# Kernel tuning notes

Measured on AMD Instinct MI355X. Metric: run time of the kernel, lower is better.

Reference implementation:

```python
import jax, jax.numpy as jnp
import numpy as np

B, S, HID, NH = 2, 2048, 2048, 16
DH = HID // NH  # 128


def _rope_tables(seq_len, dim, dtype=jnp.float32):
    inv_freq = 1.0 / (10000.0 ** (jnp.arange(0, dim, 2, dtype=jnp.float32) / dim))
    t = jnp.arange(seq_len, dtype=jnp.float32)
    freqs = jnp.einsum('i,j->ij', t, inv_freq)          # [S, dim/2]
    emb = jnp.concatenate([freqs, freqs], axis=-1)       # [S, dim]
    return jnp.cos(emb)[None, None].astype(dtype), jnp.sin(emb)[None, None].astype(dtype)


def _rotate_half(x):
    x1, x2 = x[..., : x.shape[-1] // 2], x[..., x.shape[-1] // 2 :]
    return jnp.concatenate([-x2, x1], axis=-1)


def setup_inputs() -> dict:
    key = jax.random.key(0)
    ks = jax.random.split(key, 6)
    hidden_states = jax.random.normal(ks[0], (B, S, HID), dtype=jnp.float32)
    scale = 1.0 / np.sqrt(HID)
    Wq = jax.random.normal(ks[1], (HID, HID), dtype=jnp.float32) * scale
    Wk = jax.random.normal(ks[2], (HID, HID), dtype=jnp.float32) * scale
    Wv = jax.random.normal(ks[3], (HID, HID), dtype=jnp.float32) * scale
    Wo = jax.random.normal(ks[4], (HID, HID), dtype=jnp.float32) * scale
    bq = jnp.zeros((HID,), jnp.float32)
    bk = jnp.zeros((HID,), jnp.float32)
    bv = jnp.zeros((HID,), jnp.float32)
    bo = jnp.zeros((HID,), jnp.float32)
    # causal additive mask [1,1,S,S]
    causal = jnp.tril(jnp.ones((S, S), dtype=bool))
    attention_mask = jnp.where(causal, 0.0, -1e9).astype(jnp.float32)[None, None]
    return dict(hidden_states=hidden_states, attention_mask=attention_mask,
                Wq=Wq, bq=bq, Wk=Wk, bk=bk, Wv=Wv, bv=bv, Wo=Wo, bo=bo)


def reference(hidden_states, attention_mask, Wq, bq, Wk, bk, Wv, bv, Wo, bo):
    b, s, _ = hidden_states.shape
    # torch Linear: x @ W.T + b
    q = (hidden_states @ Wq.T + bq).reshape(b, s, NH, DH).transpose(0, 2, 1, 3)
    k = (hidden_states @ Wk.T + bk).reshape(b, s, NH, DH).transpose(0, 2, 1, 3)
    v = (hidden_states @ Wv.T + bv).reshape(b, s, NH, DH).transpose(0, 2, 1, 3)
    cos, sin = _rope_tables(s, DH)
    q = q * cos + _rotate_half(q) * sin
    k = k * cos + _rotate_half(k) * sin
    scores = jnp.einsum('bhqd,bhkd->bhqk', q * (DH ** -0.5), k)
    scores = scores + attention_mask
    probs = jax.nn.softmax(scores, axis=-1)  # dropout: eval mode (identity)
    out = jnp.einsum('bhqk,bhkd->bhqd', probs, v)
    out = out.transpose(0, 2, 1, 3).reshape(b, s, HID)
    return out @ Wo.T + bo
```

## Files before the change

### kernel.cpp

```cpp
#include <hip/hip_runtime.h>
#include <hip/hip_bf16.h>
#include <cstdint>
#include <cstddef>

#define BB 2
#define SS 2048
#define HH 2048
#define NHH 16
#define DHH 128

using f32x4  = __attribute__((ext_vector_type(4))) float;
using bf16x8 = __attribute__((ext_vector_type(8))) __bf16;
using bf16x4 = __attribute__((ext_vector_type(4))) __bf16;
using bfloat = __bf16;

__device__ inline void gload_lds16(const void* g, void* l) {
    __builtin_amdgcn_global_load_lds(
        (const __attribute__((address_space(1))) void*)g,
        (__attribute__((address_space(3))) void*)l, 16, 0, 0);
}

__device__ inline f32x4 mfma16(bf16x8 a, bf16x8 b, f32x4 c) {
    return __builtin_amdgcn_mfma_f32_16x16x32_bf16(a, b, c, 0, 0, 0);
}

template <int CTRL>
__device__ inline float dpp_max_step(float x) {
    int y = __builtin_amdgcn_update_dpp(0, __builtin_bit_cast(int, x), CTRL, 0xf, 0xf, false);
    return fmaxf(x, __builtin_bit_cast(float, y));
}
__device__ inline float rowmax16(float x) {
    x = dpp_max_step<0x121>(x);
    x = dpp_max_step<0x122>(x);
    x = dpp_max_step<0x124>(x);
    x = dpp_max_step<0x128>(x);
    return x;
}

__global__ void cvt_bf16(const float* __restrict__ in, bfloat* __restrict__ out, int n4) {
    int i = blockIdx.x * blockDim.x + threadIdx.x;
    if (i >= n4) return;
    float4 v = reinterpret_cast<const float4*>(in)[i];
    bf16x4 o;
    o[0] = (bfloat)v.x; o[1] = (bfloat)v.y; o[2] = (bfloat)v.z; o[3] = (bfloat)v.w;
    reinterpret_cast<bf16x4*>(out)[i] = o;
}

__global__ void cvt_bf16_w(const float* __restrict__ s0, const float* __restrict__ s1,
                           const float* __restrict__ s2, const float* __restrict__ s3,
                           bfloat* __restrict__ d0, bfloat* __restrict__ d1,
                           bfloat* __restrict__ d2, bfloat* __restrict__ d3) {
    int sel = blockIdx.x >> 12;
    int i = (blockIdx.x & 4095) * 256 + threadIdx.x;
    const float* s = sel == 0 ? s0 : sel == 1 ? s1 : sel == 2 ? s2 : s3;
    bfloat* d = sel == 0 ? d0 : sel == 1 ? d1 : sel == 2 ? d2 : d3;
    float4 v = reinterpret_cast<const float4*>(s)[i];
    bf16x4 o;
    o[0] = (bfloat)v.x; o[1] = (bfloat)v.y; o[2] = (bfloat)v.z; o[3] = (bfloat)v.w;
    reinterpret_cast<bf16x4*>(d)[i] = o;
}

__global__ void rope_table(float* __restrict__ cosT, float* __restrict__ sinT) {
    int i = blockIdx.x * blockDim.x + threadIdx.x;
    if (i >= SS * 64) return;
    int s = i >> 6, j = i & 63;
    float invf = powf(10000.0f, -(float)j / 64.0f);
    float ang = (float)s * invf;
    cosT[i] = cosf(ang);
    sinT[i] = sinf(ang);
}

__global__ __launch_bounds__(256, 2)
void gemm_qkv(const bfloat* __restrict__ A,
              const bfloat* __restrict__ Bq, const bfloat* __restrict__ Bk,
              const bfloat* __restrict__ Bv,
              const float* __restrict__ bq, const float* __restrict__ bk,
              const float* __restrict__ bv,
              bfloat* __restrict__ Qo, bfloat* __restrict__ Ko, bfloat* __restrict__ Vto,
              const float* __restrict__ cosT, const float* __restrict__ sinT) {
    constexpr int BM = 128, BN = 128, BK = 32, K = HH, N = HH;
    __shared__ bfloat As[BM * BK];
    __shared__ bfloat Bs[BN * BK];
    const int t = threadIdx.x, w = t >> 6, l = t & 63;
    const int lr = l & 15, lg = l >> 4;
    const int sel = blockIdx.y >> 4;
    const bfloat* Bt = sel == 0 ? Bq : sel == 1 ? Bk : Bv;
    const float* bias = sel == 0 ? bq : sel == 1 ? bk : bv;
    const int m0 = blockIdx.x * BM, n0 = (blockIdx.y & 15) * BN;
    const int wm = (w >> 1) * 64;
    const int base = (t & ~63) * 8;

    f32x4 acc[4][4] = {};

    for (int kb = 0; kb < K; kb += BK) {
#pragma unroll
        for (int i = 0; i < 2; i++) {
            int idx = i * 256 + t;
            int r = idx >> 2, k8 = (idx & 3) << 3;
            gload_lds16(A  + (size_t)(m0 + r) * K + kb + k8, As + (i * 2048 + base));
            gload_lds16(Bt + (size_t)(n0 + r) * K + kb + k8, Bs + (i * 2048 + base));
        }
        __syncthreads();
        bf16x8 af[4], bfr[4];
#pragma unroll
        for (int mi = 0; mi < 4; mi++)
            af[mi] = *reinterpret_cast<const bf16x8*>(&As[(wm + mi * 16 + lr) * BK + lg * 8]);
#pragma unroll
        for (int ni = 0; ni < 4; ni++) {
            int cb = (w & 1) * 32 + (ni & 1) * 16 + (ni >> 1) * 64;
            bfr[ni] = *reinterpret_cast<const bf16x8*>(&Bs[(cb + lr) * BK + lg * 8]);
        }
#pragma unroll
        for (int mi = 0; mi < 4; mi++)
#pragma unroll
            for (int ni = 0; ni < 4; ni++)
                acc[mi][ni] = mfma16(af[mi], bfr[ni], acc[mi][ni]);
        __syncthreads();
    }

    if (sel == 2) {
#pragma unroll
        for (int mi = 0; mi < 4; mi++) {
            int row = m0 + wm + mi * 16 + lg * 4;
#pragma unroll
            for (int ni = 0; ni < 4; ni++) {
                int cb = (w & 1) * 32 + (ni & 1) * 16 + (ni >> 1) * 64;
                int col = n0 + cb + lr;
                float bv_ = bias[col];
#pragma unroll
                for (int j = 0; j < 4; j++) {
                    float v = acc[mi][ni][j] + bv_;
                    int bb = (row + j) >> 11;
                    int s  = (row + j) & (SS - 1);
                    Vto[((size_t)(bb * HH + col)) * SS + s] = (bfloat)v;
                }
            }
        }
    } else {
        bfloat* C = sel == 0 ? Qo : Ko;
        const float qscale = sel == 0 ? 0.088388347648318447f : 1.0f;
#pragma unroll
        for (int mi = 0; mi < 4; mi++) {
            int row = m0 + wm + mi * 16 + lg * 4;
#pragma unroll
            for (int ni = 0; ni < 2; ni++) {
                int d = (w & 1) * 32 + ni * 16 + lr;
                int col1 = n0 + d, col2 = col1 + 64;
                float b1 = bias[col1], b2 = bias[col2];
#pragma unroll
                for (int j = 0; j < 4; j++) {
                    int s = (row + j) & (SS - 1);
                    float c  = cosT[s * 64 + d];
                    float sn = sinT[s * 64 + d];
                    float x1 = acc[mi][ni][j] + b1;
                    float x2 = acc[mi][ni + 2][j] + b2;
                    float o1 = (x1 * c - x2 * sn) * qscale;
                    float o2 = (x2 * c + x1 * sn) * qscale;
                    C[(size_t)(row + j) * N + col1] = (bfloat)o1;
                    C[(size_t)(row + j) * N + col2] = (bfloat)o2;
                }
            }
        }
    }
}

__global__ __launch_bounds__(256, 2)
void gemm_out(const bfloat* __restrict__ A, const bfloat* __restrict__ Bt,
              const float* __restrict__ bias, float* __restrict__ C,
              int M, int N, int K) {
    constexpr int BM = 128, BN = 128, BK = 32;
    __shared__ bfloat As[BM * BK];
    __shared__ bfloat Bs[BN * BK];
    const int t = threadIdx.x, w = t >> 6, l = t & 63;
    const int lr = l & 15, lg = l >> 4;
    const int m0 = blockIdx.x * BM, n0 = blockIdx.y * BN;
    const int wm = (w >> 1) * 64;
    const int base = (t & ~63) * 8;

    f32x4 acc[4][4] = {};

    for (int kb = 0; kb < K; kb += BK) {
#pragma unroll
        for (int i = 0; i < 2; i++) {
            int idx = i * 256 + t;
            int r = idx >> 2, k8 = (idx & 3) << 3;
            gload_lds16(A  + (size_t)(m0 + r) * K + kb + k8, As + (i * 2048 + base));
            gload_lds16(Bt + (size_t)(n0 + r) * K + kb + k8, Bs + (i * 2048 + base));
        }
        __syncthreads();
        bf16x8 af[4], bfr[4];
#pragma unroll
        for (int mi = 0; mi < 4; mi++)
            af[mi] = *reinterpret_cast<const bf16x8*>(&As[(wm + mi * 16 + lr) * BK + lg * 8]);
#pragma unroll
        for (int ni = 0; ni < 4; ni++) {
            int cb = (w & 1) * 32 + (ni & 1) * 16 + (ni >> 1) * 64;
            bfr[ni] = *reinterpret_cast<const bf16x8*>(&Bs[(cb + lr) * BK + lg * 8]);
        }
#pragma unroll
        for (int mi = 0; mi < 4; mi++)
#pragma unroll
            for (int ni = 0; ni < 4; ni++)
                acc[mi][ni] = mfma16(af[mi], bfr[ni], acc[mi][ni]);
        __syncthreads();
    }

#pragma unroll
    for (int mi = 0; mi < 4; mi++) {
        int row = m0 + wm + mi * 16 + lg * 4;
#pragma unroll
        for (int ni = 0; ni < 4; ni++) {
            int cb = (w & 1) * 32 + (ni & 1) * 16 + (ni >> 1) * 64;
            int col = n0 + cb + lr;
            float bv = bias[col];
#pragma unroll
            for (int j = 0; j < 4; j++)
                C[(size_t)(row + j) * N + col] = acc[mi][ni][j] + bv;
        }
    }
}

__global__ __launch_bounds__(256, 4)
void attn_fwd(const bfloat* __restrict__ Q, const bfloat* __restrict__ K,
              const bfloat* __restrict__ Vt, bfloat* __restrict__ O) {
    __shared__ bfloat Ks[64 * 128];
    __shared__ bfloat Vs[128 * 64];
    __shared__ bfloat Pw[4][16 * 64];

    const int t = threadIdx.x, w = t >> 6, l = t & 63;
    const int lr = l & 15, lg = l >> 4;
    const int swz = (lr & 7) << 4;

    const int f = blockIdx.x;
    const int xcd = f & 7, slot = f >> 3;
    const int bh = xcd + 8 * (slot >> 5);
    const int qidx = 31 - (slot & 31);
    const int b = bh >> 4, h = bh & 15;
    const int q0 = qidx * 64 + w * 16;

    const size_t bo_ = (size_t)b * SS * HH + (size_t)h * DHH;
    const bfloat* Qp = Q + bo_;
    const bfloat* Kp = K + bo_;
    const bfloat* Vp = Vt + (size_t)(b * NHH + h) * DHH * SS;
    bfloat* Op = O + bo_;

    auto stage = [&](int kv0) {
#pragma unroll
        for (int i = 0; i < 4; i++) {
            int Ub = (i * 4 + w) * 64;
            int U = Ub + l;
            int r = U >> 4;
            int u = (U & 15) ^ (r & 7);
            gload_lds16(Kp + (size_t)(kv0 + r) * HH + u * 8, &Ks[Ub * 8]);
        }
#pragma unroll
        for (int i = 0; i < 4; i++) {
            int Ub = (i * 4 + w) * 64;
            int U = Ub + l;
            int r = U >> 3;
            int u = (U & 7) ^ (r & 7);
            gload_lds16(Vp + (size_t)r * SS + kv0 + u * 8, &Vs[Ub * 8]);
        }
    };

    bf16x8 qf[4];
#pragma unroll
    for (int kt = 0; kt < 4; kt++)
        qf[kt] = *reinterpret_cast<const bf16x8*>(Qp + (size_t)(q0 + lr) * HH + kt * 32 + lg * 8);

    bf16x8 ones;
#pragma unroll
    for (int e = 0; e < 8; e++) ones[e] = (bfloat)1.0f;

    f32x4 o[8] = {};
    f32x4 lsv = {};
    float m[4];
#pragma unroll
    for (int j = 0; j < 4; j++) m[j] = -1e30f;

    const int nkv = qidx + 1;

    for (int kv = 0; kv < nkv; ++kv) {
        stage(kv * 64);
        __syncthreads();

        const char* KB = (const char*)&Ks[0];
        const char* VB = (const char*)&Vs[0];

        f32x4 sc[4] = {};
        __builtin_amdgcn_s_setprio(1);
#pragma unroll
        for (int kt = 0; kt < 4; kt++) {
            const int col = (kt * 64 + lg * 16);
#pragma unroll
            for (int kb = 0; kb < 4; kb++) {
                bf16x8 kf = *reinterpret_cast<const bf16x8*>(
                    KB + (kb * 16 + lr) * 256 + (col ^ swz));
                sc[kb] = mfma16(qf[kt], kf, sc[kb]);
            }
        }
        __builtin_amdgcn_s_setprio(0);

        const bool diag = (kv == nkv - 1);
        float p[4][4], alpha[4];
        bool ga = false;
#pragma unroll
        for (int j = 0; j < 4; j++) {
            float v0 = sc[0][j], v1 = sc[1][j], v2 = sc[2][j], v3 = sc[3][j];
            if (diag) {
                int qr = q0 + lg * 4 + j;
                int k0 = kv * 64 + lr;
                if (k0      > qr) v0 = -1e30f;
                if (k0 + 16 > qr) v1 = -1e30f;
                if (k0 + 32 > qr) v2 = -1e30f;
                if (k0 + 48 > qr) v3 = -1e30f;
            }
            float mx = rowmax16(fmaxf(fmaxf(v0, v1), fmaxf(v2, v3)));
            bool grow = mx > m[j] + 8.0f;
            float mn = grow ? mx : m[j];
            alpha[j] = grow ? __expf(m[j] - mn) : 1.0f;
            m[j] = mn;
            ga = ga || grow;
            p[0][j] = __expf(v0 - mn);
            p[1][j] = __expf(v1 - mn);
            p[2][j] = __expf(v2 - mn);
            p[3][j] = __expf(v3 - mn);
        }
        if (__any(ga)) {
#pragma unroll
            for (int j = 0; j < 4; j++) {
                lsv[j] *= alpha[j];
#pragma unroll
                for (int nt = 0; nt < 8; nt++) o[nt][j] *= alpha[j];
            }
        }

        char* pwb = (char*)&Pw[w][0];
#pragma unroll
        for (int j = 0; j < 4; j++) {
            int q = lg * 4 + j;
            int qs = (q & 7) << 4;
#pragma unroll
            for (int kb = 0; kb < 4; kb++)
                *(bfloat*)(pwb + q * 128 + ((kb * 32 + lr * 2) ^ qs)) = (bfloat)p[kb][j];
        }
        asm volatile("s_waitcnt lgkmcnt(0)" ::: "memory");
        __builtin_amdgcn_sched_barrier(0);

        const char* pwr = (const char*)&Pw[w][0];
        bf16x8 pa0 = *reinterpret_cast<const bf16x8*>(pwr + lr * 128 + ((lg * 16) ^ swz));
        bf16x8 pa1 = *reinterpret_cast<const bf16x8*>(pwr + lr * 128 + ((64 + lg * 16) ^ swz));
        __builtin_amdgcn_s_setprio(1);
        lsv = mfma16(pa0, ones, lsv);
        lsv = mfma16(pa1, ones, lsv);
#pragma unroll
        for (int nt = 0; nt < 8; nt++) {
            const char* vb = VB + (nt * 16 + lr) * 128;
            bf16x8 vf0 = *reinterpret_cast<const bf16x8*>(vb + ((lg * 16) ^ swz));
            bf16x8 vf1 = *reinterpret_cast<const bf16x8*>(vb + ((64 + lg * 16) ^ swz));
            o[nt] = mfma16(pa0, vf0, o[nt]);
            o[nt] = mfma16(pa1, vf1, o[nt]);
        }
        __builtin_amdgcn_s_setprio(0);
        __syncthreads();
    }

#pragma unroll
    for (int j = 0; j < 4; j++) {
        float inv = 1.0f / lsv[j];
        int row = q0 + lg * 4 + j;
#pragma unroll
        for (int nt = 0; nt < 8; nt++)
            Op[(size_t)row * HH + nt * 16 + lr] = (bfloat)(o[nt][j] * inv);
    }
}

extern "C" void kernel_launch(void* const* d_in, const int* in_sizes, int n_in,
                              void* d_out, int out_size, void* d_ws, size_t ws_size,
                              hipStream_t stream) {
    (void)in_sizes; (void)n_in; (void)out_size; (void)ws_size;
    const float* hs = (const float*)d_in[0];
    const float* Wq = (const float*)d_in[2];
    const float* bq = (const float*)d_in[3];
    const float* Wk = (const float*)d_in[4];
    const float* bk = (const float*)d_in[5];
    const float* Wv = (const float*)d_in[6];
    const float* bv = (const float*)d_in[7];
    const float* Wo = (const float*)d_in[8];
    const float* bo = (const float*)d_in[9];

    char* ws = (char*)d_ws;
    size_t off = 0;
    auto alloc = [&](size_t bytes) { void* p = ws + off; off += (bytes + 255) & ~(size_t)255; return p; };
    const size_t MK = (size_t)BB * SS * HH;
    const size_t NK = (size_t)HH * HH;

    bfloat* Xb  = (bfloat*)alloc(MK * 2);
    bfloat* Wqb = (bfloat*)alloc(NK * 2);
    bfloat* Wkb = (bfloat*)alloc(NK * 2);
    bfloat* Wvb = (bfloat*)alloc(NK * 2);
    bfloat* Wob = (bfloat*)alloc(NK * 2);
    bfloat* Qb  = (bfloat*)alloc(MK * 2);
    bfloat* Kb  = (bfloat*)alloc(MK * 2);
    bfloat* Vtb = (bfloat*)alloc(MK * 2);
    float*  cosT = (float*)alloc((size_t)SS * 64 * 4);
    float*  sinT = (float*)alloc((size_t)SS * 64 * 4);
    bfloat* AOb = Xb;

    cvt_bf16<<<(int)(MK / 4 / 256), 256, 0, stream>>>(hs, Xb, (int)(MK / 4));
    cvt_bf16_w<<<4 * 4096, 256, 0, stream>>>(Wq, Wk, Wv, Wo, Wqb, Wkb, Wvb, Wob);
    rope_table<<<(SS * 64 + 255) / 256, 256, 0, stream>>>(cosT, sinT);

    gemm_qkv<<<dim3(BB * SS / 128, 48), 256, 0, stream>>>(
        Xb, Wqb, Wkb, Wvb, bq, bk, bv, Qb, Kb, Vtb, cosT, sinT);

    attn_fwd<<<1024, 256, 0, stream>>>(Qb, Kb, Vtb, AOb);

    gemm_out<<<dim3(BB * SS / 128, HH / 128), 256, 0, stream>>>(
        AOb, Wob, bo, (float*)d_out, BB * SS, HH, HH);
}
```

Baseline: 308.8 us.

## Triple-buffer GEMM k-loop with 256x128 tiles, BK=64 and swizzled LDS

Replaces the single-buffered BK=32 GEMM main loop in both the QKV and output projections with a shared 3-stage pipelined k-loop. It uses 512-thread blocks computing 256x128 tiles, BK=64, and XOR-swizzled LDS layouts. Explicit vmcnt waits and barriers let global-to-LDS loads for later stages overlap the MFMA work of the current stage, and s_setprio raises priority during the MFMA burst. The cost is much more LDS per block (about 144KB), which limits occupancy, plus half as many blocks per grid.

```diff
diff --git a/kernel.cpp b/kernel.cpp
--- a/kernel.cpp
+++ b/kernel.cpp
@@ -70,7 +70,85 @@
     sinT[i] = sinf(ang);
 }
 
-__global__ __launch_bounds__(256, 2)
+__device__ __forceinline__ void kloop256(const bfloat* __restrict__ Ag,
+                                         const bfloat* __restrict__ Bg,
+                                         f32x4 (&acc)[4][4]) {
+    constexpr int K = HH, NT = K / 64;
+    __shared__ bfloat Abuf[3][256 * 64];
+    __shared__ bfloat Bbuf[3][128 * 64];
+    const int t = threadIdx.x, l = t & 63, lr = l & 15, lg = l >> 4;
+    const int wid = t >> 6, wr = wid >> 1, wc = wid & 1;
+    const int dstu = (t & ~63);
+
+    auto stage = [&](int buf, int kt) {
+#pragma unroll
+        for (int i = 0; i < 4; i++) {
+            int U = i * 512 + t, row = U >> 3, u = (U & 7) ^ (row & 7);
+            gload_lds16(Ag + (size_t)row * K + kt * 64 + u * 8,
+                        &Abuf[buf][(i * 512 + dstu) * 8]);
+        }
+#pragma unroll
+        for (int i = 0; i < 2; i++) {
+            int U = i * 512 + t, row = U >> 3, u = (U & 7) ^ (row & 7);
+            gload_lds16(Bg + (size_t)row * K + kt * 64 + u * 8,
+                        &Bbuf[buf][(i * 512 + dstu) * 8]);
+        }
+    };
+
+    int cmap[4];
+#pragma unroll
+    for (int n = 0; n < 4; n++)
+        cmap[n] = (n < 2) ? wc * 32 + n * 16 : 64 + wc * 32 + (n - 2) * 16;
+    const int usw0 = lg ^ (lr & 7);
+    const int usw1 = (4 + lg) ^ (lr & 7);
+
+    stage(0, 0);
+    stage(1, 1);
+
+#pragma unroll 1
+    for (int kt = 0; kt < NT; ++kt) {
+        const int buf = kt % 3;
+        if (kt + 2 < NT) {
+            stage((kt + 2) % 3, kt + 2);
+            asm volatile("s_waitcnt vmcnt(12)" ::: "memory");
+        } else if (kt + 1 < NT) {
+            asm volatile("s_waitcnt vmcnt(6)" ::: "memory");
+        } else {
+            asm volatile("s_waitcnt vmcnt(0)" ::: "memory");
+        }
+        __builtin_amdgcn_s_barrier();
+        __builtin_amdgcn_sched_barrier(0);
+
+        const bfloat* Ab = Abuf[buf];
+        const bfloat* Bb = Bbuf[buf];
+        bf16x8 af[4][2], bfr[4][2];
+#pragma unroll
+        for (int m = 0; m < 4; m++) {
+            int row = wr * 64 + m * 16 + lr;
+            af[m][0] = *reinterpret_cast<const bf16x8*>(&Ab[row * 64 + usw0 * 8]);
+            af[m][1] = *reinterpret_cast<const bf16x8*>(&Ab[row * 64 + usw1 * 8]);
+        }
+#pragma unroll
+        for (int n = 0; n < 4; n++) {
+            int row = cmap[n] + lr;
+            bfr[n][0] = *reinterpret_cast<const bf16x8*>(&Bb[row * 64 + usw0 * 8]);
+            bfr[n][1] = *reinterpret_cast<const bf16x8*>(&Bb[row * 64 + usw1 * 8]);
+        }
+        __builtin_amdgcn_s_setprio(1);
+#pragma unroll
+        for (int m = 0; m < 4; m++)
+#pragma unroll
+            for (int n = 0; n < 4; n++) {
+                acc[m][n] = mfma16(af[m][0], bfr[n][0], acc[m][n]);
+                acc[m][n] = mfma16(af[m][1], bfr[n][1], acc[m][n]);
+            }
+        __builtin_amdgcn_s_setprio(0);
+        __builtin_amdgcn_sched_barrier(0);
+        __builtin_amdgcn_s_barrier();
+    }
+}
+
+__global__ __launch_bounds__(512, 2)
 void gemm_qkv(const bfloat* __restrict__ A,
               const bfloat* __restrict__ Bq, const bfloat* __restrict__ Bk,
               const bfloat* __restrict__ Bv,
@@ -78,144 +156,83 @@
               const float* __restrict__ bv,
               bfloat* __restrict__ Qo, bfloat* __restrict__ Ko, bfloat* __restrict__ Vto,
               const float* __restrict__ cosT, const float* __restrict__ sinT) {
-    constexpr int BM = 128, BN = 128, BK = 32, K = HH, N = HH;
-    __shared__ bfloat As[BM * BK];
-    __shared__ bfloat Bs[BN * BK];
-    const int t = threadIdx.x, w = t >> 6, l = t & 63;
-    const int lr = l & 15, lg = l >> 4;
+    constexpr int K = HH, N = HH;
     const int sel = blockIdx.y >> 4;
     const bfloat* Bt = sel == 0 ? Bq : sel == 1 ? Bk : Bv;
     const float* bias = sel == 0 ? bq : sel == 1 ? bk : bv;
-    const int m0 = blockIdx.x * BM, n0 = (blockIdx.y & 15) * BN;
-    const int wm = (w >> 1) * 64;
-    const int base = (t & ~63) * 8;
+    const int m0 = blockIdx.x * 256, n0 = (blockIdx.y & 15) * 128;
 
     f32x4 acc[4][4] = {};
-
-    for (int kb = 0; kb < K; kb += BK) {
-#pragma unroll
-        for (int i = 0; i < 2; i++) {
-            int idx = i * 256 + t;
-            int r = idx >> 2, k8 = (idx & 3) << 3;
-            gload_lds16(A  + (size_t)(m0 + r) * K + kb + k8, As + (i * 2048 + base));
-            gload_lds16(Bt + (size_t)(n0 + r) * K + kb + k8, Bs + (i * 2048 + base));
-        }
-        __syncthreads();
-        bf16x8 af[4], bfr[4];
-#pragma unroll
-        for (int mi = 0; mi < 4; mi++)
-            af[mi] = *reinterpret_cast<const bf16x8*>(&As[(wm + mi * 16 + lr) * BK + lg * 8]);
-#pragma unroll
-        for (int ni = 0; ni < 4; ni++) {
-            int cb = (w & 1) * 32 + (ni & 1) * 16 + (ni >> 1) * 64;
-            bfr[ni] = *reinterpret_cast<const bf16x8*>(&Bs[(cb + lr) * BK + lg * 8]);
-        }
-#pragma unroll
-        for (int mi = 0; mi < 4; mi++)
-#pragma unroll
-            for (int ni = 0; ni < 4; ni++)
-                acc[mi][ni] = mfma16(af[mi], bfr[ni], acc[mi][ni]);
-        __syncthreads();
-    }
+    kloop256(A + (size_t)m0 * K, Bt + (size_t)n0 * K, acc);
+
+    const int t = threadIdx.x, l = t & 63, lr = l & 15, lg = l >> 4;
+    const int wid = t >> 6, wr = wid >> 1, wc = wid & 1;
 
     if (sel == 2) {
 #pragma unroll
-        for (int mi = 0; mi < 4; mi++) {
-            int row = m0 + wm + mi * 16 + lg * 4;
-#pragma unroll
-            for (int ni = 0; ni < 4; ni++) {
-                int cb = (w & 1) * 32 + (ni & 1) * 16 + (ni >> 1) * 64;
-                int col = n0 + cb + lr;
+        for (int m = 0; m < 4; m++) {
+            int row = m0 + wr * 64 + m * 16 + lg * 4;
+#pragma unroll
+            for (int n = 0; n < 4; n++) {
+                int cm = (n < 2) ? wc * 32 + n * 16 : 64 + wc * 32 + (n - 2) * 16;
+                int col = n0 + cm + lr;
                 float bv_ = bias[col];
 #pragma unroll
                 for (int j = 0; j < 4; j++) {
-                    float v = acc[mi][ni][j] + bv_;
-                    int bb = (row + j) >> 11;
-                    int s  = (row + j) & (SS - 1);
-                    Vto[((size_t)(bb * HH + col)) * SS + s] = (bfloat)v;
+                    int r = row + j;
+                    Vto[((size_t)((r >> 11) * HH + col)) * SS + (r & (SS - 1))] =
+                        (bfloat)(acc[m][n][j] + bv_);
                 }
             }
         }
     } else {
         bfloat* C = sel == 0 ? Qo : Ko;
-        const float qscale = sel == 0 ? 0.088388347648318447f : 1.0f;
-#pragma unroll
-        for (int mi = 0; mi < 4; mi++) {
-            int row = m0 + wm + mi * 16 + lg * 4;
-#pragma unroll
-            for (int ni = 0; ni < 2; ni++) {
-                int d = (w & 1) * 32 + ni * 16 + lr;
+        const float qs = sel == 0 ? 0.088388347648318447f : 1.0f;
+#pragma unroll
+        for (int m = 0; m < 4; m++) {
+            int row = m0 + wr * 64 + m * 16 + lg * 4;
+#pragma unroll
+            for (int n = 0; n < 2; n++) {
+                int d = wc * 32 + n * 16 + lr;
                 int col1 = n0 + d, col2 = col1 + 64;
                 float b1 = bias[col1], b2 = bias[col2];
 #pragma unroll
                 for (int j = 0; j < 4; j++) {
-                    int s = (row + j) & (SS - 1);
+                    int r = row + j, s = r & (SS - 1);
                     float c  = cosT[s * 64 + d];
                     float sn = sinT[s * 64 + d];
-                    float x1 = acc[mi][ni][j] + b1;
-                    float x2 = acc[mi][ni + 2][j] + b2;
-                    float o1 = (x1 * c - x2 * sn) * qscale;
-                    float o2 = (x2 * c + x1 * sn) * qscale;
-                    C[(size_t)(row + j) * N + col1] = (bfloat)o1;
-                    C[(size_t)(row + j) * N + col2] = (bfloat)o2;
+                    float x1 = acc[m][n][j] + b1;
+                    float x2 = acc[m][n + 2][j] + b2;
+                    C[(size_t)r * N + col1] = (bfloat)((x1 * c - x2 * sn) * qs);
+                    C[(size_t)r * N + col2] = (bfloat)((x2 * c + x1 * sn) * qs);
                 }
             }
         }
     }
 }
 
-__global__ __launch_bounds__(256, 2)
+__global__ __launch_bounds__(512, 2)
 void gemm_out(const bfloat* __restrict__ A, const bfloat* __restrict__ Bt,
-              const float* __restrict__ bias, float* __restrict__ C,
-              int M, int N, int K) {
-    constexpr int BM = 128, BN = 128, BK = 32;
-    __shared__ bfloat As[BM * BK];
-    __shared__ bfloat Bs[BN * BK];
-    const int t = threadIdx.x, w = t >> 6, l = t & 63;
-    const int lr = l & 15, lg = l >> 4;
-    const int m0 = blockIdx.x * BM, n0 = blockIdx.y * BN;
-    const int wm = (w >> 1) * 64;
-    const int base = (t & ~63) * 8;
+              const float* __restrict__ bias, float* __restrict__ C) {
+    constexpr int K = HH, N = HH;
+    const int m0 = blockIdx.x * 256, n0 = blockIdx.y * 128;
 
     f32x4 acc[4][4] = {};
-
-    for (int kb = 0; kb < K; kb += BK) {
-#pragma unroll
-        for (int i = 0; i < 2; i++) {
-            int idx = i * 256 + t;
-            int r = idx >> 2, k8 = (idx & 3) << 3;
-            gload_lds16(A  + (size_t)(m0 + r) * K + kb + k8, As + (i * 2048 + base));
-            gload_lds16(Bt + (size_t)(n0 + r) * K + kb + k8, Bs + (i * 2048 + base));
-        }
-        __syncthreads();
-        bf16x8 af[4], bfr[4];
-#pragma unroll
-        for (int mi = 0; mi < 4; mi++)
-            af[mi] = *reinterpret_cast<const bf16x8*>(&As[(wm + mi * 16 + lr) * BK + lg * 8]);
-#pragma unroll
-        for (int ni = 0; ni < 4; ni++) {
-            int cb = (w & 1) * 32 + (ni & 1) * 16 + (ni >> 1) * 64;
-            bfr[ni] = *reinterpret_cast<const bf16x8*>(&Bs[(cb + lr) * BK + lg * 8]);
-        }
-#pragma unroll
-        for (int mi = 0; mi < 4; mi++)
-#pragma unroll
-            for (int ni = 0; ni < 4; ni++)
-                acc[mi][ni] = mfma16(af[mi], bfr[ni], acc[mi][ni]);
-        __syncthreads();
-    }
-
-#pragma unroll
-    for (int mi = 0; mi < 4; mi++) {
-        int row = m0 + wm + mi * 16 + lg * 4;
-#pragma unroll
-        for (int ni = 0; ni < 4; ni++) {
-            int cb = (w & 1) * 32 + (ni & 1) * 16 + (ni >> 1) * 64;
-            int col = n0 + cb + lr;
+    kloop256(A + (size_t)m0 * K, Bt + (size_t)n0 * K, acc);
+
+    const int t = threadIdx.x, l = t & 63, lr = l & 15, lg = l >> 4;
+    const int wid = t >> 6, wr = wid >> 1, wc = wid & 1;
+#pragma unroll
+    for (int m = 0; m < 4; m++) {
+        int row = m0 + wr * 64 + m * 16 + lg * 4;
+#pragma unroll
+        for (int n = 0; n < 4; n++) {
+            int cm = (n < 2) ? wc * 32 + n * 16 : 64 + wc * 32 + (n - 2) * 16;
+            int col = n0 + cm + lr;
             float bv = bias[col];
 #pragma unroll
             for (int j = 0; j < 4; j++)
-                C[(size_t)(row + j) * N + col] = acc[mi][ni][j] + bv;
+                C[(size_t)(row + j) * N + col] = acc[m][n][j] + bv;
         }
     }
 }
@@ -411,11 +428,11 @@
     cvt_bf16_w<<<4 * 4096, 256, 0, stream>>>(Wq, Wk, Wv, Wo, Wqb, Wkb, Wvb, Wob);
     rope_table<<<(SS * 64 + 255) / 256, 256, 0, stream>>>(cosT, sinT);
 
-    gemm_qkv<<<dim3(BB * SS / 128, 48), 256, 0, stream>>>(
+    gemm_qkv<<<dim3(BB * SS / 256, 48), 512, 0, stream>>>(
         Xb, Wqb, Wkb, Wvb, bq, bk, bv, Qb, Kb, Vtb, cosT, sinT);
 
     attn_fwd<<<1024, 256, 0, stream>>>(Qb, Kb, Vtb, AOb);
 
-    gemm_out<<<dim3(BB * SS / 128, HH / 128), 256, 0, stream>>>(
-        AOb, Wob, bo, (float*)d_out, BB * SS, HH, HH);
-}
+    gemm_out<<<dim3(BB * SS / 256, HH / 128), 512, 0, stream>>>(
+        AOb, Wob, bo, (float*)d_out);
+}
```

Result: no change. 311.1 us (+0.7%).

## Double-buffer GEMM K-loop with swizzled LDS and shared pipelined helper

Applied to the files above, without the earlier changes.

Both projection GEMMs now share one K-loop helper. It double-buffers the A and B tiles in LDS, prefetching the next K-tile with direct global-to-LDS loads while the current tile feeds the MFMAs, and waits with explicit vmcnt counts instead of two full syncs per iteration. LDS chunks are XOR-swizzled to reduce bank conflicts on fragment reads, and MFMA issue is wrapped in setprio. Launch bounds rise to 4 waves/SIMD occupancy, and the doubled LDS footprint (32KB per block) still fits that.

```diff
diff --git a/kernel.cpp b/kernel.cpp
--- a/kernel.cpp
+++ b/kernel.cpp
@@ -70,7 +70,77 @@
     sinT[i] = sinf(ang);
 }
 
-__global__ __launch_bounds__(256, 2)
+__device__ __forceinline__ void kloop128(const bfloat* __restrict__ Ag,
+                                         const bfloat* __restrict__ Bg,
+                                         f32x4 (&acc)[4][4]) {
+    constexpr int K = HH, NT = K / 32;
+    __shared__ bfloat As[2][128 * 32];
+    __shared__ bfloat Bs[2][128 * 32];
+    const int t = threadIdx.x, l = t & 63, lr = l & 15, lg = l >> 4;
+    const int w = t >> 6, wm = (w >> 1) * 64, wc = w & 1;
+    const int ubase = t & ~63;
+
+    auto stage = [&](int buf, int kt) {
+#pragma unroll
+        for (int i = 0; i < 2; i++) {
+            int idx = i * 256 + t;
+            int r = idx >> 2, u = idx & 3;
+            int us = u ^ (r & 3) ^ ((r >> 2) & 1);
+            gload_lds16(Ag + (size_t)r * K + kt * 32 + us * 8,
+                        &As[buf][(i * 256 + ubase) * 8]);
+        }
+#pragma unroll
+        for (int i = 0; i < 2; i++) {
+            int idx = i * 256 + t;
+            int r = idx >> 2, u = idx & 3;
+            int us = u ^ (r & 3) ^ ((r >> 2) & 1);
+            gload_lds16(Bg + (size_t)r * K + kt * 32 + us * 8,
+                        &Bs[buf][(i * 256 + ubase) * 8]);
+        }
+    };
+
+    stage(0, 0);
+
+#pragma unroll 1
+    for (int kt = 0; kt < NT; ++kt) {
+        const int buf = kt & 1;
+        if (kt + 1 < NT) {
+            stage(buf ^ 1, kt + 1);
+            asm volatile("s_waitcnt vmcnt(4)" ::: "memory");
+        } else {
+            asm volatile("s_waitcnt vmcnt(0)" ::: "memory");
+        }
+        __builtin_amdgcn_s_barrier();
+        __builtin_amdgcn_sched_barrier(0);
+
+        const bfloat* A_ = As[buf];
+        const bfloat* B_ = Bs[buf];
+        bf16x8 af[4], bfr[4];
+#pragma unroll
+        for (int mi = 0; mi < 4; mi++) {
+            int row = wm + mi * 16 + lr;
+            int us = lg ^ (row & 3) ^ ((row >> 2) & 1);
+            af[mi] = *reinterpret_cast<const bf16x8*>(&A_[row * 32 + us * 8]);
+        }
+#pragma unroll
+        for (int ni = 0; ni < 4; ni++) {
+            int row = wc * 32 + (ni & 1) * 16 + (ni >> 1) * 64 + lr;
+            int us = lg ^ (row & 3) ^ ((row >> 2) & 1);
+            bfr[ni] = *reinterpret_cast<const bf16x8*>(&B_[row * 32 + us * 8]);
+        }
+        __builtin_amdgcn_s_setprio(1);
+#pragma unroll
+        for (int mi = 0; mi < 4; mi++)
+#pragma unroll
+            for (int ni = 0; ni < 4; ni++)
+                acc[mi][ni] = mfma16(af[mi], bfr[ni], acc[mi][ni]);
+        __builtin_amdgcn_s_setprio(0);
+        __builtin_amdgcn_sched_barrier(0);
+        __builtin_amdgcn_s_barrier();
+    }
+}
+
+__global__ __launch_bounds__(256, 4)
 void gemm_qkv(const bfloat* __restrict__ A,
               const bfloat* __restrict__ Bq, const bfloat* __restrict__ Bk,
               const bfloat* __restrict__ Bv,
@@ -78,45 +148,17 @@
               const float* __restrict__ bv,
               bfloat* __restrict__ Qo, bfloat* __restrict__ Ko, bfloat* __restrict__ Vto,
               const float* __restrict__ cosT, const float* __restrict__ sinT) {
-    constexpr int BM = 128, BN = 128, BK = 32, K = HH, N = HH;
-    __shared__ bfloat As[BM * BK];
-    __shared__ bfloat Bs[BN * BK];
-    const int t = threadIdx.x, w = t >> 6, l = t & 63;
-    const int lr = l & 15, lg = l >> 4;
+    constexpr int K = HH, N = HH;
     const int sel = blockIdx.y >> 4;
     const bfloat* Bt = sel == 0 ? Bq : sel == 1 ? Bk : Bv;
     const float* bias = sel == 0 ? bq : sel == 1 ? bk : bv;
-    const int m0 = blockIdx.x * BM, n0 = (blockIdx.y & 15) * BN;
-    const int wm = (w >> 1) * 64;
-    const int base = (t & ~63) * 8;
+    const int m0 = blockIdx.x * 128, n0 = (blockIdx.y & 15) * 128;
 
     f32x4 acc[4][4] = {};
-
-    for (int kb = 0; kb < K; kb += BK) {
-#pragma unroll
-        for (int i = 0; i < 2; i++) {
-            int idx = i * 256 + t;
-            int r = idx >> 2, k8 = (idx & 3) << 3;
-            gload_lds16(A  + (size_t)(m0 + r) * K + kb + k8, As + (i * 2048 + base));
-            gload_lds16(Bt + (size_t)(n0 + r) * K + kb + k8, Bs + (i * 2048 + base));
-        }
-        __syncthreads();
-        bf16x8 af[4], bfr[4];
-#pragma unroll
-        for (int mi = 0; mi < 4; mi++)
-            af[mi] = *reinterpret_cast<const bf16x8*>(&As[(wm + mi * 16 + lr) * BK + lg * 8]);
-#pragma unroll
-        for (int ni = 0; ni < 4; ni++) {
-            int cb = (w & 1) * 32 + (ni & 1) * 16 + (ni >> 1) * 64;
-            bfr[ni] = *reinterpret_cast<const bf16x8*>(&Bs[(cb + lr) * BK + lg * 8]);
-        }
-#pragma unroll
-        for (int mi = 0; mi < 4; mi++)
-#pragma unroll
-            for (int ni = 0; ni < 4; ni++)
-                acc[mi][ni] = mfma16(af[mi], bfr[ni], acc[mi][ni]);
-        __syncthreads();
-    }
+    kloop128(A + (size_t)m0 * K, Bt + (size_t)n0 * K, acc);
+
+    const int t = threadIdx.x, l = t & 63, lr = l & 15, lg = l >> 4;
+    const int w = t >> 6, wm = (w >> 1) * 64, wc = w & 1;
 
     if (sel == 2) {
 #pragma unroll
@@ -124,93 +166,60 @@
             int row = m0 + wm + mi * 16 + lg * 4;
 #pragma unroll
             for (int ni = 0; ni < 4; ni++) {
-                int cb = (w & 1) * 32 + (ni & 1) * 16 + (ni >> 1) * 64;
+                int cb = wc * 32 + (ni & 1) * 16 + (ni >> 1) * 64;
                 int col = n0 + cb + lr;
                 float bv_ = bias[col];
 #pragma unroll
                 for (int j = 0; j < 4; j++) {
-                    float v = acc[mi][ni][j] + bv_;
-                    int bb = (row + j) >> 11;
-                    int s  = (row + j) & (SS - 1);
-                    Vto[((size_t)(bb * HH + col)) * SS + s] = (bfloat)v;
+                    int r = row + j;
+                    Vto[((size_t)((r >> 11) * HH + col)) * SS + (r & (SS - 1))] =
+                        (bfloat)(acc[mi][ni][j] + bv_);
                 }
             }
         }
     } else {
         bfloat* C = sel == 0 ? Qo : Ko;
-        const float qscale = sel == 0 ? 0.088388347648318447f : 1.0f;
+        const float qs = sel == 0 ? 0.088388347648318447f : 1.0f;
 #pragma unroll
         for (int mi = 0; mi < 4; mi++) {
             int row = m0 + wm + mi * 16 + lg * 4;
 #pragma unroll
             for (int ni = 0; ni < 2; ni++) {
-                int d = (w & 1) * 32 + ni * 16 + lr;
+                int d = wc * 32 + ni * 16 + lr;
                 int col1 = n0 + d, col2 = col1 + 64;
                 float b1 = bias[col1], b2 = bias[col2];
 #pragma unroll
                 for (int j = 0; j < 4; j++) {
-                    int s = (row + j) & (SS - 1);
+                    int r = row + j, s = r & (SS - 1);
                     float c  = cosT[s * 64 + d];
                     float sn = sinT[s * 64 + d];
                     float x1 = acc[mi][ni][j] + b1;
                     float x2 = acc[mi][ni + 2][j] + b2;
-                    float o1 = (x1 * c - x2 * sn) * qscale;
-                    float o2 = (x2 * c + x1 * sn) * qscale;
-                    C[(size_t)(row + j) * N + col1] = (bfloat)o1;
-                    C[(size_t)(row + j) * N + col2] = (bfloat)o2;
+                    C[(size_t)r * N + col1] = (bfloat)((x1 * c - x2 * sn) * qs);
+                    C[(size_t)r * N + col2] = (bfloat)((x2 * c + x1 * sn) * qs);
                 }
             }
         }
     }
 }
 
-__global__ __launch_bounds__(256, 2)
+__global__ __launch_bounds__(256, 4)
 void gemm_out(const bfloat* __restrict__ A, const bfloat* __restrict__ Bt,
-              const float* __restrict__ bias, float* __restrict__ C,
-              int M, int N, int K) {
-    constexpr int BM = 128, BN = 128, BK = 32;
-    __shared__ bfloat As[BM * BK];
-    __shared__ bfloat Bs[BN * BK];
-    const int t = threadIdx.x, w = t >> 6, l = t & 63;
-    const int lr = l & 15, lg = l >> 4;
-    const int m0 = blockIdx.x * BM, n0 = blockIdx.y * BN;
-    const int wm = (w >> 1) * 64;
-    const int base = (t & ~63) * 8;
+              const float* __restrict__ bias, float* __restrict__ C) {
+    constexpr int K = HH, N = HH;
+    const int m0 = blockIdx.x * 128, n0 = blockIdx.y * 128;
 
     f32x4 acc[4][4] = {};
-
-    for (int kb = 0; kb < K; kb += BK) {
-#pragma unroll
-        for (int i = 0; i < 2; i++) {
-            int idx = i * 256 + t;
-            int r = idx >> 2, k8 = (idx & 3) << 3;
-            gload_lds16(A  + (size_t)(m0 + r) * K + kb + k8, As + (i * 2048 + base));
-            gload_lds16(Bt + (size_t)(n0 + r) * K + kb + k8, Bs + (i * 2048 + base));
-        }
-        __syncthreads();
-        bf16x8 af[4], bfr[4];
-#pragma unroll
-        for (int mi = 0; mi < 4; mi++)
-            af[mi] = *reinterpret_cast<const bf16x8*>(&As[(wm + mi * 16 + lr) * BK + lg * 8]);
-#pragma unroll
-        for (int ni = 0; ni < 4; ni++) {
-            int cb = (w & 1) * 32 + (ni & 1) * 16 + (ni >> 1) * 64;
-            bfr[ni] = *reinterpret_cast<const bf16x8*>(&Bs[(cb + lr) * BK + lg * 8]);
-        }
-#pragma unroll
-        for (int mi = 0; mi < 4; mi++)
-#pragma unroll
-            for (int ni = 0; ni < 4; ni++)
-                acc[mi][ni] = mfma16(af[mi], bfr[ni], acc[mi][ni]);
-        __syncthreads();
-    }
-
+    kloop128(A + (size_t)m0 * K, Bt + (size_t)n0 * K, acc);
+
+    const int t = threadIdx.x, l = t & 63, lr = l & 15, lg = l >> 4;
+    const int w = t >> 6, wm = (w >> 1) * 64, wc = w & 1;
 #pragma unroll
     for (int mi = 0; mi < 4; mi++) {
         int row = m0 + wm + mi * 16 + lg * 4;
 #pragma unroll
         for (int ni = 0; ni < 4; ni++) {
-            int cb = (w & 1) * 32 + (ni & 1) * 16 + (ni >> 1) * 64;
+            int cb = wc * 32 + (ni & 1) * 16 + (ni >> 1) * 64;
             int col = n0 + cb + lr;
             float bv = bias[col];
 #pragma unroll
@@ -417,5 +426,5 @@
     attn_fwd<<<1024, 256, 0, stream>>>(Qb, Kb, Vtb, AOb);
 
     gemm_out<<<dim3(BB * SS / 128, HH / 128), 256, 0, stream>>>(
-        AOb, Wob, bo, (float*)d_out, BB * SS, HH, HH);
-}
+        AOb, Wob, bo, (float*)d_out);
+}
```

Result: no change. 310.9 us (+0.7%).
